# Kernel tuning notes

Hardware: AMD Instinct MI355X
Metric: run time of the kernel (lower is better)

Reference implementation:

```python
import jax, jax.numpy as jnp
import numpy as np

N_SIDE = 7
N_NODES = N_SIDE * N_SIDE  # 49


def _grid_edge_index(h, w):
    # torch_geometric.utils.grid: 9-point stencil (8 neighbors + self-loop)
    src, dst = [], []
    for y in range(h):
        for x in range(w):
            for dy in (-1, 0, 1):
                for dx in (-1, 0, 1):
                    ny, nx = y + dy, x + dx
                    if 0 <= ny < h and 0 <= nx < w:
                        src.append(ny * w + nx)
                        dst.append(y * w + x)
    return np.stack([np.array(src), np.array(dst)]).astype(np.int64)


def _gcn_norm_adj(edge_index, n):
    # PyG GCNConv default: add self-loops (on top of any existing), weight 1,
    # deg = in-degree by edge weight, A_hat = D^-1/2 (A + I) D^-1/2
    src, dst = edge_index[0], edge_index[1]
    A = jnp.zeros((n, n), dtype=jnp.float32).at[dst, src].add(1.0)
    A = A + jnp.eye(n, dtype=jnp.float32)  # GCNConv's added self-loops
    deg = A.sum(axis=1)
    d_inv_sqrt = jnp.where(deg > 0, jax.lax.rsqrt(deg), 0.0)
    return A * d_inv_sqrt[:, None] * d_inv_sqrt[None, :]  # [n, n]


def setup_inputs() -> dict:
    key = jax.random.key(0)
    ks = jax.random.split(key, 4)
    B = 4096
    features = jax.random.normal(ks[0], (B, N_NODES, 768), dtype=jnp.float32)
    W1 = jax.random.normal(ks[1], (768, 256), dtype=jnp.float32) * (1.0 / np.sqrt(768))
    b1 = jnp.zeros((256,), dtype=jnp.float32)
    W2 = jax.random.normal(ks[2], (256, 128), dtype=jnp.float32) * (1.0 / np.sqrt(256))
    b2 = jnp.zeros((128,), dtype=jnp.float32)
    fcW = jax.random.normal(ks[3], (128, 4), dtype=jnp.float32) * (1.0 / np.sqrt(128))
    fcb = jnp.zeros((4,), dtype=jnp.float32)
    edge_index = jnp.asarray(_grid_edge_index(N_SIDE, N_SIDE))  # [2, 361]
    return {"features": features, "W1": W1, "b1": b1, "W2": W2, "b2": b2,
            "fcW": fcW, "fcb": fcb, "edge_index": edge_index}


def reference(features, W1, b1, W2, b2, fcW, fcb, edge_index):
    # features: [B, N, 768]; batched GCN over the shared 7x7 grid graph
    A_hat = _gcn_norm_adj(edge_index, N_NODES)  # [N, N]
    # GCNConv: aggregate(X @ W) + b
    h = jnp.einsum('mn,bnd->bmd', A_hat, features @ W1) + b1  # [B, N, 256]
    h = jax.nn.relu(h)
    h = jnp.einsum('mn,bnd->bmd', A_hat, h @ W2) + b2  # [B, N, 128]
    h = jax.nn.relu(h)
    pooled = h.mean(axis=1)  # [B, 128] mean over nodes
    return pooled @ fcW + fcb  # [B, 4]
```

## Files before the change

### kernel.cpp

```cpp
#include <hip/hip_runtime.h>

#define NN 49
#define D0 768
#define D1 256
#define D2 128

typedef short v8s __attribute__((ext_vector_type(8)));
typedef float v4f __attribute__((ext_vector_type(4)));
typedef int   v4i __attribute__((ext_vector_type(4)));

__device__ __forceinline__ unsigned short f2bf(float f) {
  unsigned int u = __float_as_uint(f);
  u += 0x7FFFu + ((u >> 16) & 1u);
  return (unsigned short)(u >> 16);
}
__device__ __forceinline__ float bf2f(unsigned short u) {
  return __uint_as_float((unsigned)u << 16);
}

__device__ __forceinline__ int permk(int k) {
  return (k & ~31) | ((k & 12) << 1) | ((k & 16) >> 2) | (k & 3);
}

__device__ __forceinline__ float ahat(int m, int k) {
  if (m >= NN || k >= NN) return 0.f;
  int ym = m / 7, xm = m % 7, yk = k / 7, xk = k % 7;
  int dy = ym - yk, dx = xm - xk;
  if (dy < -1 || dy > 1 || dx < -1 || dx > 1) return 0.f;
  float rm = rsqrtf((float)((1 + (ym > 0) + (ym < 6)) * (1 + (xm > 0) + (xm < 6))) + 1.0f);
  float rk = rsqrtf((float)((1 + (yk > 0) + (yk < 6)) * (1 + (xk > 0) + (xk < 6))) + 1.0f);
  return ((m == k) ? 2.0f : 1.0f) * rm * rk;
}

#define W1_IMG_BYTES 393216
#define WS_NEEDED    458752

__global__ void prep_w(const float* __restrict__ W1, const float* __restrict__ W2,
                       char* __restrict__ wimg) {
  int id = blockIdx.x * 256 + threadIdx.x;
  if (id < 24576) {
    int p = (id >> 8) & 7, tt = id & 255;
    int wvv = tt >> 6, lnn = tt & 63, qq = lnn >> 4, lmm = lnn & 15;
    int nt = p >> 1, s = p & 1;
    int n  = 64 * wvv + 16 * nt + lmm;
    int k0 = (id >> 11) * 64 + 32 * s + 4 * qq;
    v8s v;
    #pragma unroll
    for (int i = 0; i < 4; ++i) {
      v[i]     = (short)f2bf(W1[(size_t)(k0 + i) * D1 + n]);
      v[i + 4] = (short)f2bf(W1[(size_t)(k0 + 16 + i) * D1 + n]);
    }
    *(v8s*)(wimg + (size_t)id * 16) = v;
  }
  int id2 = id - 24576;
  if (id2 >= 0 && id2 < 4096) {
    int p = (id2 >> 8) & 3, tt = id2 & 255;
    int wvv = tt >> 6, lnn = tt & 63, qq = lnn >> 4, lmm = lnn & 15;
    int nt = p >> 1, s = p & 1;
    int n  = 32 * wvv + 16 * nt + lmm;
    int k0 = (id2 >> 10) * 64 + 32 * s + 4 * qq;
    v8s v;
    #pragma unroll
    for (int i = 0; i < 4; ++i) {
      v[i]     = (short)f2bf(W2[(size_t)(k0 + i) * D2 + n]);
      v[i + 4] = (short)f2bf(W2[(size_t)(k0 + 16 + i) * D2 + n]);
    }
    *(v8s*)(wimg + W1_IMG_BYTES + (size_t)id2 * 16) = v;
  }
}

#define SX0    0
#define SX1    8192
#define SH1_0  16384
#define SH1_1  49152
#define SPOOL0 0
#define SPOOL1 512
#define NSMEM7 81920

__device__ __forceinline__ void ldw8(v8s* dst, const char* base) {
  #pragma unroll
  for (int p = 0; p < 8; ++p) dst[p] = *(const v8s*)(base + p * 4096);
}
__device__ __forceinline__ void ldw4(v8s* dst, const char* base) {
  #pragma unroll
  for (int p = 0; p < 4; ++p) dst[p] = *(const v8s*)(base + p * 4096);
}
__device__ __forceinline__ void commit8(char* lds, const float4& a, const float4& b) {
  v8s v;
  v[0] = (short)f2bf(a.x); v[1] = (short)f2bf(a.y);
  v[2] = (short)f2bf(a.z); v[3] = (short)f2bf(a.w);
  v[4] = (short)f2bf(b.x); v[5] = (short)f2bf(b.y);
  v[6] = (short)f2bf(b.z); v[7] = (short)f2bf(b.w);
  *(v8s*)lds = v;
}

__global__ __launch_bounds__(256, 2) void gcn_fused8(
    const float* __restrict__ X, const char* __restrict__ wimg,
    const float* __restrict__ b1v, const float* __restrict__ b2v,
    const float* __restrict__ fcWv, const float* __restrict__ fcbv,
    float* __restrict__ out)
{
  __shared__ __align__(16) char smem[NSMEM7];
  const int t  = threadIdx.x;
  const int wv = t >> 6;
  const int ln = t & 63;
  const int q  = ln >> 4;
  const int lm = ln & 15;

  if (t < 240) {
    int i = (t >= 120) ? t - 120 : t;
    int base = ((t >= 120) ? SX1 : SX0) + 6272 + i * 16;
    *(v4i*)(smem + base) = (v4i){0, 0, 0, 0};
  }

  const float* X0 = X + (size_t)(2 * blockIdx.x) * (NN * D0);
  const float* X1 = X0 + NN * D0;

  const int g1 = t + 256;
  const int b1g = (g1 >= 392) ? 1 : 0;
  const bool act3 = (t < 16);
  const int s0 = t, s1 = g1 - 392 * b1g, s2 = t + 120, s3 = t + 376;
  const int r0 = s0 >> 3, f0 = s0 & 7;
  const int r1 = s1 >> 3, f1 = s1 & 7;
  const int r2 = s2 >> 3, f2 = s2 & 7;
  const int r3 = s3 >> 3, f3 = s3 & 7;
  const float* base0 = X0 + r0 * D0 + 32 * (f0 >> 2) + 4 * (f0 & 3);
  const float* base1 = (b1g ? X1 : X0) + r1 * D0 + 32 * (f1 >> 2) + 4 * (f1 & 3);
  const float* base2 = X1 + r2 * D0 + 32 * (f2 >> 2) + 4 * (f2 & 3);
  const float* base3_ = X1 + r3 * D0 + 32 * (f3 >> 2) + 4 * (f3 & 3);
  const float* base3 = act3 ? base3_ : base0;
  const int lds0 = SX0 + ((r0 * 128 + 16 * f0) ^ ((r0 & 7) << 4));
  const int lds1 = (b1g ? SX1 : SX0) + ((r1 * 128 + 16 * f1) ^ ((r1 & 7) << 4));
  const int lds2 = SX1 + ((r2 * 128 + 16 * f2) ^ ((r2 & 7) << 4));
  const int lds3 = SX1 + (((r3 & 63) * 128 + 16 * f3) ^ ((r3 & 7) << 4));

  const int tofs = t * 16;

  v4f accA[4][4], accB[4][4];
  #pragma unroll
  for (int i = 0; i < 4; ++i)
    #pragma unroll
    for (int j = 0; j < 4; ++j) {
      accA[i][j] = (v4f){0.f, 0.f, 0.f, 0.f};
      accB[i][j] = (v4f){0.f, 0.f, 0.f, 0.f};
    }

  v8s wA[8];
  ldw8(wA, wimg + tofs);
  float4 p0a = *(const float4*)(base0);
  float4 p0b = *(const float4*)(base0 + 16);
  float4 p1a = *(const float4*)(base1);
  float4 p1b = *(const float4*)(base1 + 16);
  float4 p2a = *(const float4*)(base2);
  float4 p2b = *(const float4*)(base2 + 16);
  float4 p3a = *(const float4*)(base3);
  float4 p3b = *(const float4*)(base3 + 16);

  for (int kc = 0; kc < 12; ++kc) {
    __builtin_amdgcn_sched_barrier(0);
    __builtin_amdgcn_s_barrier();
    __builtin_amdgcn_sched_barrier(0);
    commit8((char*)smem + lds0, p0a, p0b);
    commit8((char*)smem + lds1, p1a, p1b);
    commit8((char*)smem + lds2, p2a, p2b);
    if (act3) commit8((char*)smem + lds3, p3a, p3b);
    if (kc < 11) {
      const int o = (kc + 1) * 64;
      p0a = *(const float4*)(base0 + o);
      p0b = *(const float4*)(base0 + o + 16);
      p1a = *(const float4*)(base1 + o);
      p1b = *(const float4*)(base1 + o + 16);
      p2a = *(const float4*)(base2 + o);
      p2b = *(const float4*)(base2 + o + 16);
      p3a = *(const float4*)(base3 + o);
      p3b = *(const float4*)(base3 + o + 16);
    }
    __builtin_amdgcn_sched_barrier(0);
    asm volatile("s_waitcnt lgkmcnt(0)" ::: "memory");
    __builtin_amdgcn_s_barrier();
    __builtin_amdgcn_sched_barrier(0);
    #pragma unroll
    for (int ks = 0; ks < 2; ++ks) {
      const int off = ks * 64 + (q << 4);
      v8s af[4];
      #pragma unroll
      for (int mt = 0; mt < 4; ++mt) {
        int row = mt * 16 + lm;
        af[mt] = *(const v8s*)(smem + SX0 + ((row * 128 + off) ^ ((row & 7) << 4)));
      }
      #pragma unroll
      for (int mt = 0; mt < 4; ++mt)
        #pragma unroll
        for (int nt = 0; nt < 4; ++nt)
          accA[mt][nt] = __builtin_amdgcn_mfma_f32_16x16x32_bf16(af[mt], wA[2 * nt + ks], accA[mt][nt], 0, 0, 0);
    }
    #pragma unroll
    for (int ks = 0; ks < 2; ++ks) {
      const int off = ks * 64 + (q << 4);
      v8s af[4];
      #pragma unroll
      for (int mt = 0; mt < 4; ++mt) {
        int row = mt * 16 + lm;
        af[mt] = *(const v8s*)(smem + SX1 + ((row * 128 + off) ^ ((row & 7) << 4)));
      }
      #pragma unroll
      for (int mt = 0; mt < 4; ++mt)
        #pragma unroll
        for (int nt = 0; nt < 4; ++nt)
          accB[mt][nt] = __builtin_amdgcn_mfma_f32_16x16x32_bf16(af[mt], wA[2 * nt + ks], accB[mt][nt], 0, 0, 0);
    }
    if (kc < 11) ldw8(wA, wimg + (kc + 1) * 32768 + tofs);
  }

  v8s bA[2][4], bB[2][4];
  #pragma unroll
  for (int s2 = 0; s2 < 2; ++s2)
    #pragma unroll
    for (int nt = 0; nt < 4; ++nt) {
      v8s a, b;
      #pragma unroll
      for (int i = 0; i < 4; ++i) {
        a[i]     = (short)f2bf(accA[2 * s2][nt][i]);
        a[i + 4] = (short)f2bf(accA[2 * s2 + 1][nt][i]);
        b[i]     = (short)f2bf(accB[2 * s2][nt][i]);
        b[i + 4] = (short)f2bf(accB[2 * s2 + 1][nt][i]);
      }
      bA[s2][nt] = a; bB[s2][nt] = b;
    }

  float bi[4];
  #pragma unroll
  for (int nt = 0; nt < 4; ++nt) bi[nt] = b1v[64 * wv + 16 * nt + lm];

  v8s afH[4][2], afL[4][2];
  #pragma unroll
  for (int mt = 0; mt < 4; ++mt) {
    int m = 16 * mt + lm;
    #pragma unroll
    for (int s2 = 0; s2 < 2; ++s2) {
      v8s hi, lo;
      #pragma unroll
      for (int j = 0; j < 8; ++j) {
        int k = 32 * s2 + ((j & 4) << 2) + 4 * q + (j & 3);
        float v = ahat(m, k);
        unsigned short h = f2bf(v);
        hi[j] = (short)h;
        lo[j] = (short)f2bf(v - bf2f(h));
      }
      afH[mt][s2] = hi; afL[mt][s2] = lo;
    }
  }

  #pragma unroll
  for (int bb = 0; bb < 2; ++bb) {
    v4f ag[4][4];
    #pragma unroll
    for (int mt = 0; mt < 4; ++mt)
      #pragma unroll
      for (int nt = 0; nt < 4; ++nt)
        ag[mt][nt] = (v4f){bi[nt], bi[nt], bi[nt], bi[nt]};
    #pragma unroll
    for (int s2 = 0; s2 < 2; ++s2)
      #pragma unroll
      for (int nt = 0; nt < 4; ++nt) {
        v8s b = (bb == 0) ? bA[s2][nt] : bB[s2][nt];
        #pragma unroll
        for (int mt = 0; mt < 4; ++mt) {
          ag[mt][nt] = __builtin_amdgcn_mfma_f32_16x16x32_bf16(afL[mt][s2], b, ag[mt][nt], 0, 0, 0);
          ag[mt][nt] = __builtin_amdgcn_mfma_f32_16x16x32_bf16(afH[mt][s2], b, ag[mt][nt], 0, 0, 0);
        }
      }
    const int hbase = (bb == 0) ? SH1_0 : SH1_1;
    #pragma unroll
    for (int mt = 0; mt < 4; ++mt)
      #pragma unroll
      for (int nt = 0; nt < 4; ++nt) {
        int ch  = 64 * wv + 16 * nt + lm;
        int chb = 2 * permk(ch);
        #pragma unroll
        for (int r = 0; r < 4; ++r) {
          int row = 16 * mt + 4 * q + r;
          float hv = fmaxf(ag[mt][nt][r], 0.f);
          int byte = (row * 512 + chb) ^ ((row & 7) << 4);
          *(unsigned short*)(smem + hbase + byte) = f2bf(hv);
        }
      }
  }

  const char* w2img = wimg + W1_IMG_BYTES;
  v8s w2c0[4], w2c1[4], w2c2[4], w2c3[4];
  ldw4(w2c0, w2img + tofs);
  ldw4(w2c1, w2img + 16384 + tofs);
  ldw4(w2c2, w2img + 2 * 16384 + tofs);
  ldw4(w2c3, w2img + 3 * 16384 + tofs);

  __builtin_amdgcn_sched_barrier(0);
  asm volatile("s_waitcnt lgkmcnt(0)" ::: "memory");
  __builtin_amdgcn_s_barrier();
  __builtin_amdgcn_sched_barrier(0);

  float b2i0 = b2v[32 * wv + lm];
  float b2i1 = b2v[32 * wv + 16 + lm];

  #pragma unroll
  for (int bb = 0; bb < 2; ++bb) {
    const int hbase = (bb == 0) ? SH1_0 : SH1_1;
    v4f acc3[4][2];
    #pragma unroll
    for (int i = 0; i < 4; ++i) {
      acc3[i][0] = (v4f){0.f, 0.f, 0.f, 0.f};
      acc3[i][1] = (v4f){0.f, 0.f, 0.f, 0.f};
    }
    #pragma unroll
    for (int kc = 0; kc < 4; ++kc)
      #pragma unroll
      for (int ks = 0; ks < 2; ++ks) {
        const int off = ks * 64 + (q << 4);
        v8s af[4];
        #pragma unroll
        for (int mt = 0; mt < 4; ++mt) {
          int row = mt * 16 + lm;
          int byte = (row * 512 + kc * 128 + off) ^ ((row & 7) << 4);
          af[mt] = *(const v8s*)(smem + hbase + byte);
        }
        const v8s* wc = (kc == 0) ? w2c0 : (kc == 1) ? w2c1 : (kc == 2) ? w2c2 : w2c3;
        #pragma unroll
        for (int mt = 0; mt < 4; ++mt)
          #pragma unroll
          for (int nt = 0; nt < 2; ++nt)
            acc3[mt][nt] = __builtin_amdgcn_mfma_f32_16x16x32_bf16(af[mt], wc[2 * nt + ks], acc3[mt][nt], 0, 0, 0);
      }
    v4f a2[4][2];
    #pragma unroll
    for (int mt = 0; mt < 4; ++mt) {
      a2[mt][0] = (v4f){b2i0, b2i0, b2i0, b2i0};
      a2[mt][1] = (v4f){b2i1, b2i1, b2i1, b2i1};
    }
    #pragma unroll
    for (int s2 = 0; s2 < 2; ++s2)
      #pragma unroll
      for (int nt = 0; nt < 2; ++nt) {
        v8s b;
        #pragma unroll
        for (int i = 0; i < 4; ++i) {
          b[i]     = (short)f2bf(acc3[2 * s2][nt][i]);
          b[i + 4] = (short)f2bf(acc3[2 * s2 + 1][nt][i]);
        }
        #pragma unroll
        for (int mt = 0; mt < 4; ++mt) {
          a2[mt][nt] = __builtin_amdgcn_mfma_f32_16x16x32_bf16(afL[mt][s2], b, a2[mt][nt], 0, 0, 0);
          a2[mt][nt] = __builtin_amdgcn_mfma_f32_16x16x32_bf16(afH[mt][s2], b, a2[mt][nt], 0, 0, 0);
        }
      }
    float ps0 = 0.f, ps1 = 0.f;
    #pragma unroll
    for (int mt = 0; mt < 3; ++mt)
      #pragma unroll
      for (int r = 0; r < 4; ++r) {
        ps0 += fmaxf(a2[mt][0][r], 0.f);
        ps1 += fmaxf(a2[mt][1][r], 0.f);
      }
    if (q == 0) {
      ps0 += fmaxf(a2[3][0][0], 0.f);
      ps1 += fmaxf(a2[3][1][0], 0.f);
    }
    ps0 += __shfl_xor(ps0, 16); ps0 += __shfl_xor(ps0, 32);
    ps1 += __shfl_xor(ps1, 16); ps1 += __shfl_xor(ps1, 32);
    float* spool = (float*)(smem + ((bb == 0) ? SPOOL0 : SPOOL1));
    if (q == 0) {
      spool[32 * wv + lm]      = ps0 * (1.0f / 49.0f);
      spool[32 * wv + 16 + lm] = ps1 * (1.0f / 49.0f);
    }
  }
  __syncthreads();
  if (t < 8) {
    int bb = t >> 2, c = t & 3;
    const float* spool = (const float*)(smem + ((bb == 0) ? SPOOL0 : SPOOL1));
    float a = fcbv[c];
    for (int d = 0; d < D2; ++d) a += spool[d] * fcWv[d * 4 + c];
    out[(size_t)(2 * blockIdx.x + bb) * 4 + c] = a;
  }
}

#define OFF_SX    0
#define OFF_SWT   8192
#define OFF_SC    0
#define OFF_SWT2  0
#define OFF_SPOOL 25872
#define OFF_SPF   30096
#define OFF_SH1   40960
#define OFF_NBRW  73728
#define OFF_NBRI  75492
#define OFF_B1    77256
#define OFF_B2    78280
#define OFF_FCW   78792
#define OFF_FCB   80840
#define SMEM_SZ   80856

__global__ __launch_bounds__(256, 2) void gcn_fused_fb(
    const float* __restrict__ X, const float* __restrict__ W1,
    const float* __restrict__ b1v, const float* __restrict__ W2,
    const float* __restrict__ b2v, const float* __restrict__ fcWv,
    const float* __restrict__ fcbv, float* __restrict__ out)
{
  __shared__ __align__(16) char smem[SMEM_SZ];
  const int t  = threadIdx.x;
  const int wv = t >> 6;
  const int ln = t & 63;
  const int q  = ln >> 4;
  const int lm = ln & 15;

  float* nbrW = (float*)(smem + OFF_NBRW);
  int*   nbrI = (int*)  (smem + OFF_NBRI);
  float* b1s  = (float*)(smem + OFF_B1);
  float* b2s  = (float*)(smem + OFF_B2);
  float* fcWs = (float*)(smem + OFF_FCW);
  float* fcbs = (float*)(smem + OFF_FCB);
  float* sC   = (float*)(smem + OFF_SC);

  if (t < D1) b1s[t] = b1v[t];
  if (t < D2) b2s[t] = b2v[t];
  fcWs[t]       = fcWv[t];
  fcWs[t + 256] = fcWv[t + 256];
  if (t < 4) fcbs[t] = fcbv[t];
  if (t < NN) {
    int y = t / 7, x = t % 7;
    float rm = rsqrtf((float)((1 + (y > 0) + (y < 6)) * (1 + (x > 0) + (x < 6))) + 1.0f);
    int cnt = 0;
    for (int dy = -1; dy <= 1; ++dy)
      for (int dx = -1; dx <= 1; ++dx) {
        int ny = y + dy, nx = x + dx;
        if (ny >= 0 && ny < 7 && nx >= 0 && nx < 7) {
          int n = ny * 7 + nx;
          float rn = rsqrtf((float)((1 + (ny > 0) + (ny < 6)) * (1 + (nx > 0) + (nx < 6))) + 1.0f);
          nbrW[t * 9 + cnt] = ((n == t) ? 2.0f : 1.0f) * rm * rn;
          nbrI[t * 9 + cnt] = n;
          ++cnt;
        }
      }
    for (; cnt < 9; ++cnt) { nbrW[t * 9 + cnt] = 0.0f; nbrI[t * 9 + cnt] = 0; }
  }
  __syncthreads();

  const float* Xb = X + (size_t)blockIdx.x * (NN * D0);
  v4f acc[4][4];
  #pragma unroll
  for (int i = 0; i < 4; ++i)
    #pragma unroll
    for (int j = 0; j < 4; ++j)
      acc[i][j] = (v4f){0.f, 0.f, 0.f, 0.f};

  for (int kc = 0; kc < 12; ++kc) {
    __syncthreads();
    #pragma unroll
    for (int p = 0; p < 4; ++p) {
      int idx = t + 256 * p;
      int row = idx >> 4;
      int k4  = (idx & 15) << 2;
      float4 v = {0.f, 0.f, 0.f, 0.f};
      if (row < NN) v = *(const float4*)(Xb + row * D0 + kc * 64 + k4);
      ushort4 s;
      s.x = f2bf(v.x); s.y = f2bf(v.y); s.z = f2bf(v.z); s.w = f2bf(v.w);
      int byte = row * 128 + 2 * permk(k4);
      byte ^= (row & 7) << 4;
      *(ushort4*)(smem + OFF_SX + byte) = s;
    }
    #pragma unroll
    for (int p = 0; p < 4; ++p) {
      int bid2 = t + 256 * p;
      int k0 = (bid2 & 15) << 2;
      int n0 = (bid2 >> 4) << 2;
      const float* wp = W1 + (size_t)(kc * 64 + k0) * D1 + n0;
      float4 r0 = *(const float4*)(wp);
      float4 r1 = *(const float4*)(wp + D1);
      float4 r2 = *(const float4*)(wp + 2 * D1);
      float4 r3 = *(const float4*)(wp + 3 * D1);
      int kb = 2 * permk(k0);
      ushort4 s; int byte;
      s.x = f2bf(r0.x); s.y = f2bf(r1.x); s.z = f2bf(r2.x); s.w = f2bf(r3.x);
      byte = (n0 + 0) * 128 + kb; byte ^= ((n0 + 0) & 7) << 4;
      *(ushort4*)(smem + OFF_SWT + byte) = s;
      s.x = f2bf(r0.y); s.y = f2bf(r1.y); s.z = f2bf(r2.y); s.w = f2bf(r3.y);
      byte = (n0 + 1) * 128 + kb; byte ^= ((n0 + 1) & 7) << 4;
      *(ushort4*)(smem + OFF_SWT + byte) = s;
      s.x = f2bf(r0.z); s.y = f2bf(r1.z); s.z = f2bf(r2.z); s.w = f2bf(r3.z);
      byte = (n0 + 2) * 128 + kb; byte ^= ((n0 + 2) & 7) << 4;
      *(ushort4*)(smem + OFF_SWT + byte) = s;
      s.x = f2bf(r0.w); s.y = f2bf(r1.w); s.z = f2bf(r2.w); s.w = f2bf(r3.w);
      byte = (n0 + 3) * 128 + kb; byte ^= ((n0 + 3) & 7) << 4;
      *(ushort4*)(smem + OFF_SWT + byte) = s;
    }
    __syncthreads();
    #pragma unroll
    for (int ks = 0; ks < 2; ++ks) {
      int off = ks * 64 + (q << 4);
      v8s af[4], bf[4];
      #pragma unroll
      for (int mt = 0; mt < 4; ++mt) {
        int row = mt * 16 + lm;
        int byte = row * 128 + off; byte ^= (row & 7) << 4;
        af[mt] = *(const v8s*)(smem + OFF_SX + byte);
      }
      #pragma unroll
      for (int nt = 0; nt < 4; ++nt) {
        int n = (wv * 4 + nt) * 16 + lm;
        int byte = n * 128 + off; byte ^= (n & 7) << 4;
        bf[nt] = *(const v8s*)(smem + OFF_SWT + byte);
      }
      #pragma unroll
      for (int mt = 0; mt < 4; ++mt)
        #pragma unroll
        for (int nt = 0; nt < 4; ++nt)
          acc[mt][nt] = __builtin_amdgcn_mfma_f32_16x16x32_bf16(af[mt], bf[nt], acc[mt][nt], 0, 0, 0);
    }
  }

  #pragma unroll
  for (int h = 0; h < 2; ++h) {
    __syncthreads();
    if ((wv >> 1) == h) {
      #pragma unroll
      for (int mt = 0; mt < 4; ++mt) {
        int rbase = mt * 16 + (q << 2);
        #pragma unroll
        for (int nt = 0; nt < 4; ++nt) {
          int c = ((wv & 1) * 4 + nt) * 16 + lm;
          #pragma unroll
          for (int r = 0; r < 4; ++r) {
            int row = rbase + r;
            if (row < NN) sC[row * 132 + c] = acc[mt][nt][r];
          }
        }
      }
    }
    __syncthreads();
    for (int p = 0; p < 7; ++p) {
      int idx = t + 256 * p;
      if (idx < NN * 32) {
        int m  = idx >> 5;
        int d4 = (idx & 31) << 2;
        int dg = h * 128 + d4;
        float a0 = b1s[dg], a1 = b1s[dg + 1], a2 = b1s[dg + 2], a3 = b1s[dg + 3];
        #pragma unroll
        for (int e = 0; e < 9; ++e) {
          float w = nbrW[m * 9 + e];
          int   n = nbrI[m * 9 + e];
          float4 cv = *(const float4*)(sC + n * 132 + d4);
          a0 += w * cv.x; a1 += w * cv.y; a2 += w * cv.z; a3 += w * cv.w;
        }
        a0 = fmaxf(a0, 0.f); a1 = fmaxf(a1, 0.f); a2 = fmaxf(a2, 0.f); a3 = fmaxf(a3, 0.f);
        ushort4 s; s.x = f2bf(a0); s.y = f2bf(a1); s.z = f2bf(a2); s.w = f2bf(a3);
        int byte = m * 512 + 2 * permk(dg);
        byte ^= (m & 7) << 4;
        *(ushort4*)(smem + OFF_SH1 + byte) = s;
      }
    }
  }

  v4f acc2[4][2];
  #pragma unroll
  for (int i = 0; i < 4; ++i) { acc2[i][0] = (v4f){0.f,0.f,0.f,0.f}; acc2[i][1] = (v4f){0.f,0.f,0.f,0.f}; }

  for (int kc = 0; kc < 4; ++kc) {
    __syncthreads();
    #pragma unroll
    for (int p = 0; p < 2; ++p) {
      int bid2 = t + 256 * p;
      int k0 = (bid2 & 15) << 2;
      int n0 = (bid2 >> 4) << 2;
      const float* wp = W2 + (size_t)(kc * 64 + k0) * D2 + n0;
      float4 r0 = *(const float4*)(wp);
      float4 r1 = *(const float4*)(wp + D2);
      float4 r2 = *(const float4*)(wp + 2 * D2);
      float4 r3 = *(const float4*)(wp + 3 * D2);
      int kb = 2 * permk(k0);
      ushort4 s; int byte;
      s.x = f2bf(r0.x); s.y = f2bf(r1.x); s.z = f2bf(r2.x); s.w = f2bf(r3.x);
      byte = (n0 + 0) * 128 + kb; byte ^= ((n0 + 0) & 7) << 4;
      *(ushort4*)(smem + OFF_SWT2 + byte) = s;
      s.x = f2bf(r0.y); s.y = f2bf(r1.y); s.z = f2bf(r2.y); s.w = f2bf(r3.y);
      byte = (n0 + 1) * 128 + kb; byte ^= ((n0 + 1) & 7) << 4;
      *(ushort4*)(smem + OFF_SWT2 + byte) = s;
      s.x = f2bf(r0.z); s.y = f2bf(r1.z); s.z = f2bf(r2.z); s.w = f2bf(r3.z);
      byte = (n0 + 2) * 128 + kb; byte ^= ((n0 + 2) & 7) << 4;
      *(ushort4*)(smem + OFF_SWT2 + byte) = s;
      s.x = f2bf(r0.w); s.y = f2bf(r1.w); s.z = f2bf(r2.w); s.w = f2bf(r3.w);
      byte = (n0 + 3) * 128 + kb; byte ^= ((n0 + 3) & 7) << 4;
      *(ushort4*)(smem + OFF_SWT2 + byte) = s;
    }
    __syncthreads();
    #pragma unroll
    for (int ks = 0; ks < 2; ++ks) {
      int off = ks * 64 + (q << 4);
      v8s af[4], bf2[2];
      #pragma unroll
      for (int mt = 0; mt < 4; ++mt) {
        int row = mt * 16 + lm;
        int byte = row * 512 + kc * 128 + off; byte ^= (row & 7) << 4;
        af[mt] = *(const v8s*)(smem + OFF_SH1 + byte);
      }
      #pragma unroll
      for (int nt = 0; nt < 2; ++nt) {
        int n = (wv * 2 + nt) * 16 + lm;
        int byte = n * 128 + off; byte ^= (n & 7) << 4;
        bf2[nt] = *(const v8s*)(smem + OFF_SWT2 + byte);
      }
      #pragma unroll
      for (int mt = 0; mt < 4; ++mt)
        #pragma unroll
        for (int nt = 0; nt < 2; ++nt)
          acc2[mt][nt] = __builtin_amdgcn_mfma_f32_16x16x32_bf16(af[mt], bf2[nt], acc2[mt][nt], 0, 0, 0);
    }
  }

  __syncthreads();
  #pragma unroll
  for (int mt = 0; mt < 4; ++mt) {
    int rbase = mt * 16 + (q << 2);
    #pragma unroll
    for (int nt = 0; nt < 2; ++nt) {
      int c = (wv * 2 + nt) * 16 + lm;
      #pragma unroll
      for (int r = 0; r < 4; ++r) {
        int row = rbase + r;
        if (row < NN) sC[row * 132 + c] = acc2[mt][nt][r];
      }
    }
  }
  __syncthreads();
  {
    int d4 = (t & 31) << 2;
    int g  = t >> 5;
    float p0 = 0.f, p1 = 0.f, p2 = 0.f, p3 = 0.f;
    int m0 = g * 7, m1 = (g * 7 + 7 < NN) ? (g * 7 + 7) : NN;
    for (int m = m0; m < m1; ++m) {
      float a0 = b2s[d4], a1 = b2s[d4 + 1], a2 = b2s[d4 + 2], a3 = b2s[d4 + 3];
      #pragma unroll
      for (int e = 0; e < 9; ++e) {
        float w = nbrW[m * 9 + e];
        int   n = nbrI[m * 9 + e];
        float4 cv = *(const float4*)(sC + n * 132 + d4);
        a0 += w * cv.x; a1 += w * cv.y; a2 += w * cv.z; a3 += w * cv.w;
      }
      p0 += fmaxf(a0, 0.f); p1 += fmaxf(a1, 0.f); p2 += fmaxf(a2, 0.f); p3 += fmaxf(a3, 0.f);
    }
    float* sp = (float*)(smem + OFF_SPOOL) + g * 132 + d4;
    sp[0] = p0; sp[1] = p1; sp[2] = p2; sp[3] = p3;
  }
  __syncthreads();
  if (t < D2) {
    const float* sp = (const float*)(smem + OFF_SPOOL);
    float s = 0.f;
    #pragma unroll
    for (int g = 0; g < 8; ++g) s += sp[g * 132 + t];
    ((float*)(smem + OFF_SPF))[t] = s * (1.0f / 49.0f);
  }
  __syncthreads();
  if (t < 4) {
    const float* pf = (const float*)(smem + OFF_SPF);
    float a = fcbs[t];
    for (int d = 0; d < D2; ++d) a += pf[d] * fcWs[d * 4 + t];
    out[(size_t)blockIdx.x * 4 + t] = a;
  }
}

extern "C" void kernel_launch(void* const* d_in, const int* in_sizes, int n_in,
                              void* d_out, int out_size, void* d_ws, size_t ws_size,
                              hipStream_t stream) {
  const float* X   = (const float*)d_in[0];
  const float* W1  = (const float*)d_in[1];
  const float* b1  = (const float*)d_in[2];
  const float* W2  = (const float*)d_in[3];
  const float* b2  = (const float*)d_in[4];
  const float* fcW = (const float*)d_in[5];
  const float* fcb = (const float*)d_in[6];
  float* out = (float*)d_out;
  int B = in_sizes[0] / (NN * D0);
  if (d_ws != nullptr && ws_size >= (size_t)WS_NEEDED && (B % 2) == 0) {
    prep_w<<<112, 256, 0, stream>>>(W1, W2, (char*)d_ws);
    gcn_fused8<<<B / 2, 256, 0, stream>>>(X, (const char*)d_ws, b1, b2, fcW, fcb, out);
  } else {
    gcn_fused_fb<<<B, 256, 0, stream>>>(X, W1, b1, W2, b2, fcW, fcb, out);
  }
}
```

Measured before the change: 185.1 us.

## Split X staging into two halves overlapped with the two graph-batch MFMA phases

```diff
diff --git a/kernel.cpp b/kernel.cpp
--- a/kernel.cpp
+++ b/kernel.cpp
@@ -93,8 +93,14 @@
   v[6] = (short)f2bf(b.z); v[7] = (short)f2bf(b.w);
   *(v8s*)lds = v;
 }
-
-__global__ __launch_bounds__(256, 2) void gcn_fused8(
+#define PHASE_END  do {                                        \
+    __builtin_amdgcn_sched_barrier(0);                         \
+    asm volatile("s_waitcnt lgkmcnt(0)" ::: "memory");         \
+    __builtin_amdgcn_s_barrier();                              \
+    __builtin_amdgcn_sched_barrier(0);                         \
+  } while (0)
+
+__global__ __launch_bounds__(256, 2) void gcn_fused9(
     const float* __restrict__ X, const char* __restrict__ wimg,
     const float* __restrict__ b1v, const float* __restrict__ b2v,
     const float* __restrict__ fcWv, const float* __restrict__ fcbv,
@@ -156,29 +162,52 @@
   float4 p3a = *(const float4*)(base3);
   float4 p3b = *(const float4*)(base3 + 16);
 
+  commit8((char*)smem + lds0, p0a, p0b);
+  if (!b1g) commit8((char*)smem + lds1, p1a, p1b);
+  {
+    p0a = *(const float4*)(base0 + 64);
+    p0b = *(const float4*)(base0 + 64 + 16);
+    if (!b1g) {
+      p1a = *(const float4*)(base1 + 64);
+      p1b = *(const float4*)(base1 + 64 + 16);
+    }
+  }
+  PHASE_END;
+
   for (int kc = 0; kc < 12; ++kc) {
-    __builtin_amdgcn_sched_barrier(0);
-    __builtin_amdgcn_s_barrier();
-    __builtin_amdgcn_sched_barrier(0);
-    commit8((char*)smem + lds0, p0a, p0b);
-    commit8((char*)smem + lds1, p1a, p1b);
+    #pragma unroll
+    for (int ks = 0; ks < 2; ++ks) {
+      const int off = ks * 64 + (q << 4);
+      v8s af[4];
+      #pragma unroll
+      for (int mt = 0; mt < 4; ++mt) {
+        int row = mt * 16 + lm;
+        af[mt] = *(const v8s*)(smem + SX0 + ((row * 128 + off) ^ ((row & 7) << 4)));
+      }
+      #pragma unroll
+      for (int mt = 0; mt < 4; ++mt)
+        #pragma unroll
+        for (int nt = 0; nt < 4; ++nt)
+          accA[mt][nt] = __builtin_amdgcn_mfma_f32_16x16x32_bf16(af[mt], wA[2 * nt + ks], accA[mt][nt], 0, 0, 0);
+    }
+    if (b1g) commit8((char*)smem + lds1, p1a, p1b);
     commit8((char*)smem + lds2, p2a, p2b);
     if (act3) commit8((char*)smem + lds3, p3a, p3b);
     if (kc < 11) {
       const int o = (kc + 1) * 64;
-      p0a = *(const float4*)(base0 + o);
-      p0b = *(const float4*)(base0 + o + 16);
-      p1a = *(const float4*)(base1 + o);
-      p1b = *(const float4*)(base1 + o + 16);
+      if (b1g) {
+        p1a = *(const float4*)(base1 + o);
+        p1b = *(const float4*)(base1 + o + 16);
+      }
       p2a = *(const float4*)(base2 + o);
       p2b = *(const float4*)(base2 + o + 16);
-      p3a = *(const float4*)(base3 + o);
-      p3b = *(const float4*)(base3 + o + 16);
-    }
-    __builtin_amdgcn_sched_barrier(0);
-    asm volatile("s_waitcnt lgkmcnt(0)" ::: "memory");
-    __builtin_amdgcn_s_barrier();
-    __builtin_amdgcn_sched_barrier(0);
+      if (act3) {
+        p3a = *(const float4*)(base3 + o);
+        p3b = *(const float4*)(base3 + o + 16);
+      }
+    }
+    PHASE_END;
+
     #pragma unroll
     for (int ks = 0; ks < 2; ++ks) {
       const int off = ks * 64 + (q << 4);
@@ -186,21 +215,6 @@
       #pragma unroll
       for (int mt = 0; mt < 4; ++mt) {
         int row = mt * 16 + lm;
-        af[mt] = *(const v8s*)(smem + SX0 + ((row * 128 + off) ^ ((row & 7) << 4)));
-      }
-      #pragma unroll
-      for (int mt = 0; mt < 4; ++mt)
-        #pragma unroll
-        for (int nt = 0; nt < 4; ++nt)
-          accA[mt][nt] = __builtin_amdgcn_mfma_f32_16x16x32_bf16(af[mt], wA[2 * nt + ks], accA[mt][nt], 0, 0, 0);
-    }
-    #pragma unroll
-    for (int ks = 0; ks < 2; ++ks) {
-      const int off = ks * 64 + (q << 4);
-      v8s af[4];
-      #pragma unroll
-      for (int mt = 0; mt < 4; ++mt) {
-        int row = mt * 16 + lm;
         af[mt] = *(const v8s*)(smem + SX1 + ((row * 128 + off) ^ ((row & 7) << 4)));
       }
       #pragma unroll
@@ -209,7 +223,21 @@
         for (int nt = 0; nt < 4; ++nt)
           accB[mt][nt] = __builtin_amdgcn_mfma_f32_16x16x32_bf16(af[mt], wA[2 * nt + ks], accB[mt][nt], 0, 0, 0);
     }
-    if (kc < 11) ldw8(wA, wimg + (kc + 1) * 32768 + tofs);
+    if (kc < 11) {
+      commit8((char*)smem + lds0, p0a, p0b);
+      if (!b1g) commit8((char*)smem + lds1, p1a, p1b);
+      if (kc < 10) {
+        const int o = (kc + 2) * 64;
+        p0a = *(const float4*)(base0 + o);
+        p0b = *(const float4*)(base0 + o + 16);
+        if (!b1g) {
+          p1a = *(const float4*)(base1 + o);
+          p1b = *(const float4*)(base1 + o + 16);
+        }
+      }
+      ldw8(wA, wimg + (kc + 1) * 32768 + tofs);
+      PHASE_END;
+    }
   }
 
   v8s bA[2][4], bB[2][4];
@@ -294,10 +322,7 @@
   ldw4(w2c2, w2img + 2 * 16384 + tofs);
   ldw4(w2c3, w2img + 3 * 16384 + tofs);
 
-  __builtin_amdgcn_sched_barrier(0);
-  asm volatile("s_waitcnt lgkmcnt(0)" ::: "memory");
-  __builtin_amdgcn_s_barrier();
-  __builtin_amdgcn_sched_barrier(0);
+  PHASE_END;
 
   float b2i0 = b2v[32 * wv + lm];
   float b2i1 = b2v[32 * wv + 16 + lm];
@@ -678,7 +703,7 @@
   int B = in_sizes[0] / (NN * D0);
   if (d_ws != nullptr && ws_size >= (size_t)WS_NEEDED && (B % 2) == 0) {
     prep_w<<<112, 256, 0, stream>>>(W1, W2, (char*)d_ws);
-    gcn_fused8<<<B / 2, 256, 0, stream>>>(X, (const char*)d_ws, b1, b2, fcW, fcb, out);
+    gcn_fused9<<<B / 2, 256, 0, stream>>>(X, (const char*)d_ws, b1, b2, fcW, fcb, out);
   } else {
     gcn_fused_fb<<<B, 256, 0, stream>>>(X, W1, b1, W2, b2, fcW, fcb, out);
   }
```

Measured after the change: 203.2 us. 9.8% more time.
